# Kernel tuning notes

Hardware: AMD Instinct MI355X
Metric: run time of the kernel (lower is better)

## Reference

```python
import jax, jax.numpy as jnp
import numpy as np

N, F, A = 50000, 128, 128

def setup_inputs() -> dict:
    key = jax.random.key(0)
    ks = jax.random.split(key, 20)
    r = lambda i, shape: jax.random.normal(ks[i], shape, dtype=jnp.float32)
    w = lambda i, shape: jax.random.normal(ks[i], shape, dtype=jnp.float32) * 0.05
    return {
        "feat": r(0, (N, F)),
        "mu": r(1, (N, F, 3)),
        "T0": r(2, (N,)),
        "T1": r(3, (N, 3)),
        "T2": r(4, (N, 3, 3)),
        "T3": r(5, (N, 3, 3, 3)),
        # denseq: Dense(F,F,swish) -> Dense(F,F). Weights stored [in,out].
        "Wq1": w(6, (F, F)), "bq1": jnp.zeros((F,), jnp.float32),
        "Wq2": w(7, (F, F)), "bq2": jnp.zeros((F,), jnp.float32),
        "WT1": w(8, (F, F)),  # dense_T1, no bias
        "WT2": w(9, (F, F)),  # dense_T2, no bias
        "WT3": w(10, (F, F)), # dense_T3, no bias
        # dense_s: Dense(F,F,swish) -> Dense(F,A)
        "Ws1": w(11, (F, F)), "bs1": jnp.zeros((F,), jnp.float32),
        "Ws2": w(12, (F, A)), "bs2": jnp.zeros((A,), jnp.float32),
        "Wv": w(13, (F, A)),  # dense_v, no bias
    }

def reference(feat, mu, T0, T1, T2, T3,
              Wq1, bq1, Wq2, bq2, WT1, WT2, WT3,
              Ws1, bs1, Ws2, bs2, Wv):
    silu = jax.nn.silu  # swish
    # M0 = denseq(feat): [N, F]
    M0 = silu(feat @ Wq1 + bq1) @ Wq2 + bq2
    # M1/M2/M3: linear over feature dim of mu [N, F, 3]
    M1 = jnp.einsum('nfc,fg->ngc', mu, WT1)
    M2 = jnp.einsum('nfc,fg->ngc', mu, WT2)
    M3 = jnp.einsum('nfc,fg->ngc', mu, WT3)
    # scalar channel
    ms = jnp.sum(M1 * T1[:, None, :], axis=-1) + T0[:, None] * M0          # T1, T0 terms
    ms = ms + jnp.einsum('nfi,nfj,nij->nf', M2, M2, T2)                    # quadrupole . T2
    ms = ms + jnp.einsum('nfi,nfj,nfk,nijk->nf', M3, M3, M3, T3)           # octupole . T3
    # vector channel [N, F, 3]
    mv = T1[:, None, :] * M0[..., None]
    mv = mv + jnp.einsum('nij,nfj->nfi', T2, M1)
    mv = mv + jnp.einsum('nijk,nfj,nfk->nfi', T3, M2, M2)
    # output projections
    mv_out = jnp.einsum('nfc,fa->nac', mv, Wv)                             # [N, A, 3]
    ms_out = silu(ms @ Ws1 + bs1) @ Ws2 + bs2                              # [N, A]
    return ms_out, mv_out
```

## Files before the change

### kernel.cpp

```cpp
#include <hip/hip_runtime.h>
#include <cstdint>

#define N_NODES 50000
#define TILE 32
#define NBLK ((N_NODES + TILE - 1) / TILE)

typedef __bf16 bf16x8 __attribute__((ext_vector_type(8)));
typedef unsigned short ushort8_t __attribute__((ext_vector_type(8)));
typedef float f32x4 __attribute__((ext_vector_type(4)));

__device__ __forceinline__ unsigned short f2bf(float x) {
  union { float f; uint32_t u; } v; v.f = x;
  uint32_t r = v.u + 0x7FFFu + ((v.u >> 16) & 1u);
  return (unsigned short)(r >> 16);
}

__device__ __forceinline__ float fast_silu(float x) {
  return x / (1.0f + __expf(-x));
}

__global__ __launch_bounds__(256) void prep_weights(
    const float* __restrict__ Wq1, const float* __restrict__ Wq2,
    const float* __restrict__ WT1, const float* __restrict__ WT2,
    const float* __restrict__ WT3, const float* __restrict__ Ws1,
    const float* __restrict__ Ws2, const float* __restrict__ Wv,
    unsigned short* __restrict__ ws) {
  int tid = blockIdx.x * 256 + threadIdx.x;
  int w = tid >> 11;
  int rest = tid & 2047;
  int c = rest >> 8;
  int kt = (rest >> 6) & 3;
  int lane = rest & 63;
  int g = (lane & 15) + 16 * c;
  int k0 = kt * 32 + (lane >> 4) * 8;
  const float* srcs[8] = {Wq1, Wq2, WT1, WT2, WT3, Ws1, Ws2, Wv};
  const float* src = srcs[w];
  union { unsigned short u[8]; uint4 v; } o;
#pragma unroll
  for (int j = 0; j < 8; ++j) o.u[j] = f2bf(src[(k0 + j) * 128 + g]);
  *(uint4*)(ws + (size_t)w * 16384 + (size_t)rest * 8) = o.v;
}

__device__ __forceinline__ bf16x8 ldB(const unsigned short* __restrict__ wg,
                                      int c, int kt, int lane) {
  return __builtin_bit_cast(
      bf16x8, *(const ushort8_t*)(wg + (((c * 4 + kt) * 64 + lane)) * 8));
}

__device__ __forceinline__ void gemm16g(const unsigned short* __restrict__ sA,
                                        const unsigned short* __restrict__ wg,
                                        int lane, int cb, f32x4 acc[2][2]) {
  const int m = lane & 15, q = lane >> 4;
  const f32x4 vzero = {0.f, 0.f, 0.f, 0.f};
#pragma unroll
  for (int rt = 0; rt < 2; ++rt)
#pragma unroll
    for (int cc = 0; cc < 2; ++cc) acc[rt][cc] = vzero;
#pragma unroll
  for (int kt = 0; kt < 4; ++kt) {
    const int k0 = q * 8 + kt * 32;
    bf16x8 a0 = __builtin_bit_cast(bf16x8, *(const ushort8_t*)(sA + m * 136 + k0));
    bf16x8 a1 = __builtin_bit_cast(bf16x8, *(const ushort8_t*)(sA + (m + 16) * 136 + k0));
#pragma unroll
    for (int cc = 0; cc < 2; ++cc) {
      bf16x8 b = ldB(wg, cb + cc, kt, lane);
      acc[0][cc] = __builtin_amdgcn_mfma_f32_16x16x32_bf16(a0, b, acc[0][cc], 0, 0, 0);
      acc[1][cc] = __builtin_amdgcn_mfma_f32_16x16x32_bf16(a1, b, acc[1][cc], 0, 0, 0);
    }
  }
}

__device__ __forceinline__ void gemm3g(const unsigned short* __restrict__ s0,
                                       const unsigned short* __restrict__ s1,
                                       const unsigned short* __restrict__ s2,
                                       const unsigned short* __restrict__ wg,
                                       int lane, int cb,
                                       f32x4 A1[2][2], f32x4 A2[2][2],
                                       f32x4 A3[2][2]) {
  const int m = lane & 15, q = lane >> 4;
  const f32x4 vzero = {0.f, 0.f, 0.f, 0.f};
#pragma unroll
  for (int rt = 0; rt < 2; ++rt)
#pragma unroll
    for (int cc = 0; cc < 2; ++cc) {
      A1[rt][cc] = vzero; A2[rt][cc] = vzero; A3[rt][cc] = vzero;
    }
#pragma unroll
  for (int kt = 0; kt < 4; ++kt) {
    const int k0 = q * 8 + kt * 32;
    bf16x8 a00 = __builtin_bit_cast(bf16x8, *(const ushort8_t*)(s0 + m * 136 + k0));
    bf16x8 a01 = __builtin_bit_cast(bf16x8, *(const ushort8_t*)(s0 + (m + 16) * 136 + k0));
    bf16x8 a10 = __builtin_bit_cast(bf16x8, *(const ushort8_t*)(s1 + m * 136 + k0));
    bf16x8 a11 = __builtin_bit_cast(bf16x8, *(const ushort8_t*)(s1 + (m + 16) * 136 + k0));
    bf16x8 a20 = __builtin_bit_cast(bf16x8, *(const ushort8_t*)(s2 + m * 136 + k0));
    bf16x8 a21 = __builtin_bit_cast(bf16x8, *(const ushort8_t*)(s2 + (m + 16) * 136 + k0));
#pragma unroll
    for (int cc = 0; cc < 2; ++cc) {
      bf16x8 b = ldB(wg, cb + cc, kt, lane);
      A1[0][cc] = __builtin_amdgcn_mfma_f32_16x16x32_bf16(a00, b, A1[0][cc], 0, 0, 0);
      A1[1][cc] = __builtin_amdgcn_mfma_f32_16x16x32_bf16(a01, b, A1[1][cc], 0, 0, 0);
      A2[0][cc] = __builtin_amdgcn_mfma_f32_16x16x32_bf16(a10, b, A2[0][cc], 0, 0, 0);
      A2[1][cc] = __builtin_amdgcn_mfma_f32_16x16x32_bf16(a11, b, A2[1][cc], 0, 0, 0);
      A3[0][cc] = __builtin_amdgcn_mfma_f32_16x16x32_bf16(a20, b, A3[0][cc], 0, 0, 0);
      A3[1][cc] = __builtin_amdgcn_mfma_f32_16x16x32_bf16(a21, b, A3[1][cc], 0, 0, 0);
    }
  }
}

__global__ __launch_bounds__(256, 2) void multipole_main(
    const float* __restrict__ feat, const float* __restrict__ mu,
    const float* __restrict__ T0g, const float* __restrict__ T1g,
    const float* __restrict__ T2g, const float* __restrict__ T3g,
    const float* __restrict__ bq1, const float* __restrict__ bq2,
    const float* __restrict__ bs1, const float* __restrict__ bs2,
    const unsigned short* __restrict__ ws, float* __restrict__ out) {
  __shared__ unsigned short sXmain[TILE * 136];
  __shared__ unsigned short sXmu[3][TILE * 136];
  __shared__ float sT[TILE][47];

  const int t = threadIdx.x;
  const int lane = t & 63, wv = t >> 6;
  const int m = lane & 15, q = lane >> 4;
  const int cb = wv * 2;
  const int nodeBase = blockIdx.x * TILE;

  {
    int node = t >> 3, f0 = (t & 7) * 16;
    int gn = nodeBase + node;
    union { unsigned short u[16]; uint4 v[2]; } buf;
    if (gn < N_NODES) {
      const float4* p = (const float4*)(feat + (size_t)gn * 128 + f0);
      float xs[16];
#pragma unroll
      for (int i = 0; i < 4; ++i) *(float4*)(xs + 4 * i) = p[i];
#pragma unroll
      for (int i = 0; i < 16; ++i) buf.u[i] = f2bf(xs[i]);
    } else {
#pragma unroll
      for (int i = 0; i < 16; ++i) buf.u[i] = 0;
    }
    uint4* dst = (uint4*)&sXmain[node * 136 + f0];
    dst[0] = buf.v[0]; dst[1] = buf.v[1];
  }

  {
    int node = t >> 3, f0 = (t & 7) * 16;
    int gn = nodeBase + node;
    union { unsigned short u[16]; uint4 v[2]; } b3[3];
    if (gn < N_NODES) {
      const float4* p = (const float4*)(mu + ((size_t)gn * 128 + f0) * 3);
      float xs[48];
#pragma unroll
      for (int i = 0; i < 12; ++i) *(float4*)(xs + 4 * i) = p[i];
#pragma unroll
      for (int i = 0; i < 16; ++i) {
        b3[0].u[i] = f2bf(xs[i * 3 + 0]);
        b3[1].u[i] = f2bf(xs[i * 3 + 1]);
        b3[2].u[i] = f2bf(xs[i * 3 + 2]);
      }
    } else {
#pragma unroll
      for (int ch = 0; ch < 3; ++ch)
#pragma unroll
        for (int i = 0; i < 16; ++i) b3[ch].u[i] = 0;
    }
#pragma unroll
    for (int ch = 0; ch < 3; ++ch) {
      uint4* dst = (uint4*)&sXmu[ch][node * 136 + f0];
      dst[0] = b3[ch].v[0]; dst[1] = b3[ch].v[1];
    }
  }

  if (t < TILE) {
    int n = nodeBase + t;
    bool val = n < N_NODES;
    float t0 = val ? T0g[n] : 0.f;
    float t1[3], t2[9], t3[27];
#pragma unroll
    for (int i = 0; i < 3; ++i) t1[i] = val ? T1g[n * 3 + i] : 0.f;
#pragma unroll
    for (int i = 0; i < 9; ++i) t2[i] = val ? T2g[n * 9 + i] : 0.f;
#pragma unroll
    for (int i = 0; i < 27; ++i) t3[i] = val ? T3g[n * 27 + i] : 0.f;
    float* Tr = sT[t];
    Tr[0] = t0;
    Tr[1] = t1[0]; Tr[2] = t1[1]; Tr[3] = t1[2];
#pragma unroll
    for (int i = 0; i < 9; ++i) Tr[4 + i] = t2[i];
    Tr[13] = t2[0]; Tr[14] = t2[1] + t2[3]; Tr[15] = t2[2] + t2[6];
    Tr[16] = t2[4]; Tr[17] = t2[5] + t2[7]; Tr[18] = t2[8];
    Tr[19] = t3[0];
    Tr[20] = t3[1] + t3[3] + t3[9];
    Tr[21] = t3[2] + t3[6] + t3[18];
    Tr[22] = t3[4] + t3[10] + t3[12];
    Tr[23] = t3[5] + t3[7] + t3[11] + t3[15] + t3[19] + t3[21];
    Tr[24] = t3[8] + t3[20] + t3[24];
    Tr[25] = t3[13];
    Tr[26] = t3[14] + t3[16] + t3[22];
    Tr[27] = t3[17] + t3[23] + t3[25];
    Tr[28] = t3[26];
#pragma unroll
    for (int i = 0; i < 3; ++i) {
      const float* b = t3 + 9 * i;
      float* d = Tr + 29 + 6 * i;
      d[0] = b[0]; d[1] = b[1] + b[3]; d[2] = b[2] + b[6];
      d[3] = b[4]; d[4] = b[5] + b[7]; d[5] = b[8];
    }
  }
  __syncthreads();

  f32x4 A1[2][2], A2[2][2], A3[2][2];
  float msv[2][2][4];
  float mvv[3][2][2][4];

  gemm16g(sXmain, ws, lane, cb, A1);
  float b0 = bq1[cb * 16 + m], b1 = bq1[cb * 16 + 16 + m];
  __syncthreads();
#pragma unroll
  for (int rt = 0; rt < 2; ++rt)
#pragma unroll
    for (int ri = 0; ri < 4; ++ri) {
      int lrow = rt * 16 + q * 4 + ri;
#pragma unroll
      for (int cc = 0; cc < 2; ++cc) {
        float h = fast_silu(A1[rt][cc][ri] + (cc ? b1 : b0));
        sXmain[lrow * 136 + (cb + cc) * 16 + m] = f2bf(h);
      }
    }
  __syncthreads();

  gemm16g(sXmain, ws + 1 * 16384, lane, cb, A1);
  {
    float bb0 = bq2[cb * 16 + m], bb1 = bq2[cb * 16 + 16 + m];
#pragma unroll
    for (int rt = 0; rt < 2; ++rt)
#pragma unroll
      for (int ri = 0; ri < 4; ++ri) {
        const float* Tr = sT[rt * 16 + q * 4 + ri];
        float t0 = Tr[0], ta = Tr[1], tb = Tr[2], tc = Tr[3];
#pragma unroll
        for (int cc = 0; cc < 2; ++cc) {
          float m0 = A1[rt][cc][ri] + (cc ? bb1 : bb0);
          msv[rt][cc][ri] = t0 * m0;
          mvv[0][rt][cc][ri] = ta * m0;
          mvv[1][rt][cc][ri] = tb * m0;
          mvv[2][rt][cc][ri] = tc * m0;
        }
      }
  }

#pragma unroll
  for (int ch = 0; ch < 3; ++ch) {
    gemm16g(sXmu[ch], ws + 2 * 16384, lane, cb, A1);
#pragma unroll
    for (int rt = 0; rt < 2; ++rt)
#pragma unroll
      for (int ri = 0; ri < 4; ++ri) {
        const float* Tr = sT[rt * 16 + q * 4 + ri];
        float t1c = Tr[1 + ch];
        float u0 = Tr[4 + 0 + ch], u1 = Tr[4 + 3 + ch], u2 = Tr[4 + 6 + ch];
#pragma unroll
        for (int cc = 0; cc < 2; ++cc) {
          float v = A1[rt][cc][ri];
          msv[rt][cc][ri] += t1c * v;
          mvv[0][rt][cc][ri] += u0 * v;
          mvv[1][rt][cc][ri] += u1 * v;
          mvv[2][rt][cc][ri] += u2 * v;
        }
      }
  }

  gemm16g(sXmu[0], ws + 4 * 16384, lane, cb, A1);
  gemm16g(sXmu[1], ws + 4 * 16384, lane, cb, A2);
  gemm16g(sXmu[2], ws + 4 * 16384, lane, cb, A3);
#pragma unroll
  for (int rt = 0; rt < 2; ++rt)
#pragma unroll
    for (int ri = 0; ri < 4; ++ri) {
      const float* Cp = sT[rt * 16 + q * 4 + ri] + 19;
      float c0 = Cp[0], c1 = Cp[1], c2 = Cp[2], c3 = Cp[3], c4 = Cp[4];
      float c5 = Cp[5], c6 = Cp[6], c7 = Cp[7], c8 = Cp[8], c9 = Cp[9];
#pragma unroll
      for (int cc = 0; cc < 2; ++cc) {
        float u0 = A1[rt][cc][ri], u1 = A2[rt][cc][ri], u2 = A3[rt][cc][ri];
        float Q0 = u0 * u0, Q1 = u0 * u1, Q2 = u0 * u2;
        float Q3 = u1 * u1, Q4 = u1 * u2, Q5 = u2 * u2;
        msv[rt][cc][ri] += c0 * (Q0 * u0) + c1 * (Q0 * u1) + c2 * (Q0 * u2) +
                           c3 * (Q1 * u1) + c4 * (Q1 * u2) + c5 * (Q2 * u2) +
                           c6 * (Q3 * u1) + c7 * (Q3 * u2) + c8 * (Q4 * u2) +
                           c9 * (Q5 * u2);
      }
    }

  gemm16g(sXmu[0], ws + 3 * 16384, lane, cb, A1);
  gemm16g(sXmu[1], ws + 3 * 16384, lane, cb, A2);
  gemm16g(sXmu[2], ws + 3 * 16384, lane, cb, A3);
#pragma unroll
  for (int rt = 0; rt < 2; ++rt)
#pragma unroll
    for (int ri = 0; ri < 4; ++ri) {
      const float* Tr = sT[rt * 16 + q * 4 + ri];
      const float* q2 = Tr + 13;
      const float* d3 = Tr + 29;
      float q20 = q2[0], q21 = q2[1], q22 = q2[2], q23 = q2[3], q24 = q2[4], q25 = q2[5];
#pragma unroll
      for (int cc = 0; cc < 2; ++cc) {
        float v0 = A1[rt][cc][ri], v1 = A2[rt][cc][ri], v2 = A3[rt][cc][ri];
        float P0 = v0 * v0, P1 = v0 * v1, P2 = v0 * v2;
        float P3 = v1 * v1, P4 = v1 * v2, P5 = v2 * v2;
        msv[rt][cc][ri] += q20 * P0 + q21 * P1 + q22 * P2 + q23 * P3 + q24 * P4 + q25 * P5;
        mvv[0][rt][cc][ri] += d3[0] * P0 + d3[1] * P1 + d3[2] * P2 + d3[3] * P3 + d3[4] * P4 + d3[5] * P5;
        mvv[1][rt][cc][ri] += d3[6] * P0 + d3[7] * P1 + d3[8] * P2 + d3[9] * P3 + d3[10] * P4 + d3[11] * P5;
        mvv[2][rt][cc][ri] += d3[12] * P0 + d3[13] * P1 + d3[14] * P2 + d3[15] * P3 + d3[16] * P4 + d3[17] * P5;
      }
    }
  __syncthreads();

#pragma unroll
  for (int rt = 0; rt < 2; ++rt)
#pragma unroll
    for (int ri = 0; ri < 4; ++ri) {
      int lrow = rt * 16 + q * 4 + ri;
#pragma unroll
      for (int cc = 0; cc < 2; ++cc) {
        int col = (cb + cc) * 16 + m;
        sXmain[lrow * 136 + col] = f2bf(msv[rt][cc][ri]);
        sXmu[0][lrow * 136 + col] = f2bf(mvv[0][rt][cc][ri]);
        sXmu[1][lrow * 136 + col] = f2bf(mvv[1][rt][cc][ri]);
        sXmu[2][lrow * 136 + col] = f2bf(mvv[2][rt][cc][ri]);
      }
    }
  __syncthreads();

  gemm16g(sXmain, ws + 5 * 16384, lane, cb, A1);
  {
    float s0 = bs1[cb * 16 + m], s1 = bs1[cb * 16 + 16 + m];
    __syncthreads();
#pragma unroll
    for (int rt = 0; rt < 2; ++rt)
#pragma unroll
      for (int ri = 0; ri < 4; ++ri) {
        int lrow = rt * 16 + q * 4 + ri;
#pragma unroll
        for (int cc = 0; cc < 2; ++cc) {
          float g = fast_silu(A1[rt][cc][ri] + (cc ? s1 : s0));
          sXmain[lrow * 136 + (cb + cc) * 16 + m] = f2bf(g);
        }
      }
  }
  __syncthreads();

  gemm16g(sXmain, ws + 6 * 16384, lane, cb, A1);
  {
    float s0 = bs2[cb * 16 + m], s1 = bs2[cb * 16 + 16 + m];
#pragma unroll
    for (int rt = 0; rt < 2; ++rt)
#pragma unroll
      for (int ri = 0; ri < 4; ++ri) {
        int grow = nodeBase + rt * 16 + q * 4 + ri;
        if (grow < N_NODES) {
#pragma unroll
          for (int cc = 0; cc < 2; ++cc) {
            int col = (cb + cc) * 16 + m;
            out[(size_t)grow * 128 + col] = A1[rt][cc][ri] + (cc ? s1 : s0);
          }
        }
      }
  }

  float* out2 = out + (size_t)N_NODES * 128;
  gemm3g(sXmu[0], sXmu[1], sXmu[2], ws + 7 * 16384, lane, cb, A1, A2, A3);
#pragma unroll
  for (int rt = 0; rt < 2; ++rt)
#pragma unroll
    for (int ri = 0; ri < 4; ++ri) {
      int grow = nodeBase + rt * 16 + q * 4 + ri;
      if (grow < N_NODES) {
#pragma unroll
        for (int cc = 0; cc < 2; ++cc) {
          int col = (cb + cc) * 16 + m;
          float* p = out2 + ((size_t)grow * 128 + col) * 3;
          p[0] = A1[rt][cc][ri];
          p[1] = A2[rt][cc][ri];
          p[2] = A3[rt][cc][ri];
        }
      }
    }
}

extern "C" void kernel_launch(void* const* d_in, const int* in_sizes, int n_in,
                              void* d_out, int out_size, void* d_ws, size_t ws_size,
                              hipStream_t stream) {
  const float* feat = (const float*)d_in[0];
  const float* mu   = (const float*)d_in[1];
  const float* T0   = (const float*)d_in[2];
  const float* T1   = (const float*)d_in[3];
  const float* T2   = (const float*)d_in[4];
  const float* T3   = (const float*)d_in[5];
  const float* Wq1  = (const float*)d_in[6];
  const float* bq1  = (const float*)d_in[7];
  const float* Wq2  = (const float*)d_in[8];
  const float* bq2  = (const float*)d_in[9];
  const float* WT1  = (const float*)d_in[10];
  const float* WT2  = (const float*)d_in[11];
  const float* WT3  = (const float*)d_in[12];
  const float* Ws1  = (const float*)d_in[13];
  const float* bs1  = (const float*)d_in[14];
  const float* Ws2  = (const float*)d_in[15];
  const float* bs2  = (const float*)d_in[16];
  const float* Wv   = (const float*)d_in[17];
  unsigned short* ws = (unsigned short*)d_ws;
  float* out = (float*)d_out;

  prep_weights<<<64, 256, 0, stream>>>(Wq1, Wq2, WT1, WT2, WT3, Ws1, Ws2, Wv, ws);
  multipole_main<<<NBLK, 256, 0, stream>>>(feat, mu, T0, T1, T2, T3,
                                           bq1, bq2, bs1, bs2, ws, out);
}
```

Before: 307.6 us.

## Batch weight loads in GEMMs, merge per-channel GEMMs, use nontemporal global access

Three ideas are combined. The GEMM helpers now load all B fragments (and, in gemm16g, all A fragments) up front so memory latency can overlap the MFMA chain. The three per-channel gemm16g calls for the WT1, WT2 and WT3 products become single gemm3g calls that share weight loads across channels, with the T1/T2 epilogue rewritten to match. Streaming input loads and output stores become nontemporal to reduce cache pollution, at the cost of more live registers, which may lower occupancy.

```diff
diff --git a/kernel.cpp b/kernel.cpp
--- a/kernel.cpp
+++ b/kernel.cpp
@@ -47,27 +47,38 @@
       bf16x8, *(const ushort8_t*)(wg + (((c * 4 + kt) * 64 + lane)) * 8));
 }
 
+__device__ __forceinline__ bf16x8 ldA(const unsigned short* __restrict__ sA,
+                                      int row, int k0) {
+  return __builtin_bit_cast(bf16x8, *(const ushort8_t*)(sA + row * 136 + k0));
+}
+
 __device__ __forceinline__ void gemm16g(const unsigned short* __restrict__ sA,
                                         const unsigned short* __restrict__ wg,
                                         int lane, int cb, f32x4 acc[2][2]) {
   const int m = lane & 15, q = lane >> 4;
-  const f32x4 vzero = {0.f, 0.f, 0.f, 0.f};
-#pragma unroll
-  for (int rt = 0; rt < 2; ++rt)
-#pragma unroll
-    for (int cc = 0; cc < 2; ++cc) acc[rt][cc] = vzero;
+  bf16x8 b[2][4], a0[4], a1[4];
+#pragma unroll
+  for (int cc = 0; cc < 2; ++cc)
+#pragma unroll
+    for (int kt = 0; kt < 4; ++kt) b[cc][kt] = ldB(wg, cb + cc, kt, lane);
 #pragma unroll
   for (int kt = 0; kt < 4; ++kt) {
     const int k0 = q * 8 + kt * 32;
-    bf16x8 a0 = __builtin_bit_cast(bf16x8, *(const ushort8_t*)(sA + m * 136 + k0));
-    bf16x8 a1 = __builtin_bit_cast(bf16x8, *(const ushort8_t*)(sA + (m + 16) * 136 + k0));
+    a0[kt] = ldA(sA, m, k0);
+    a1[kt] = ldA(sA, m + 16, k0);
+  }
+  const f32x4 vzero = {0.f, 0.f, 0.f, 0.f};
+#pragma unroll
+  for (int rt = 0; rt < 2; ++rt)
+#pragma unroll
+    for (int cc = 0; cc < 2; ++cc) acc[rt][cc] = vzero;
+#pragma unroll
+  for (int kt = 0; kt < 4; ++kt)
 #pragma unroll
     for (int cc = 0; cc < 2; ++cc) {
-      bf16x8 b = ldB(wg, cb + cc, kt, lane);
-      acc[0][cc] = __builtin_amdgcn_mfma_f32_16x16x32_bf16(a0, b, acc[0][cc], 0, 0, 0);
-      acc[1][cc] = __builtin_amdgcn_mfma_f32_16x16x32_bf16(a1, b, acc[1][cc], 0, 0, 0);
-    }
-  }
+      acc[0][cc] = __builtin_amdgcn_mfma_f32_16x16x32_bf16(a0[kt], b[cc][kt], acc[0][cc], 0, 0, 0);
+      acc[1][cc] = __builtin_amdgcn_mfma_f32_16x16x32_bf16(a1[kt], b[cc][kt], acc[1][cc], 0, 0, 0);
+    }
 }
 
 __device__ __forceinline__ void gemm3g(const unsigned short* __restrict__ s0,
@@ -78,6 +89,11 @@
                                        f32x4 A1[2][2], f32x4 A2[2][2],
                                        f32x4 A3[2][2]) {
   const int m = lane & 15, q = lane >> 4;
+  bf16x8 b[2][4];
+#pragma unroll
+  for (int cc = 0; cc < 2; ++cc)
+#pragma unroll
+    for (int kt = 0; kt < 4; ++kt) b[cc][kt] = ldB(wg, cb + cc, kt, lane);
   const f32x4 vzero = {0.f, 0.f, 0.f, 0.f};
 #pragma unroll
   for (int rt = 0; rt < 2; ++rt)
@@ -88,21 +104,20 @@
 #pragma unroll
   for (int kt = 0; kt < 4; ++kt) {
     const int k0 = q * 8 + kt * 32;
-    bf16x8 a00 = __builtin_bit_cast(bf16x8, *(const ushort8_t*)(s0 + m * 136 + k0));
-    bf16x8 a01 = __builtin_bit_cast(bf16x8, *(const ushort8_t*)(s0 + (m + 16) * 136 + k0));
-    bf16x8 a10 = __builtin_bit_cast(bf16x8, *(const ushort8_t*)(s1 + m * 136 + k0));
-    bf16x8 a11 = __builtin_bit_cast(bf16x8, *(const ushort8_t*)(s1 + (m + 16) * 136 + k0));
-    bf16x8 a20 = __builtin_bit_cast(bf16x8, *(const ushort8_t*)(s2 + m * 136 + k0));
-    bf16x8 a21 = __builtin_bit_cast(bf16x8, *(const ushort8_t*)(s2 + (m + 16) * 136 + k0));
+    bf16x8 a00 = ldA(s0, m, k0);
+    bf16x8 a01 = ldA(s0, m + 16, k0);
+    bf16x8 a10 = ldA(s1, m, k0);
+    bf16x8 a11 = ldA(s1, m + 16, k0);
+    bf16x8 a20 = ldA(s2, m, k0);
+    bf16x8 a21 = ldA(s2, m + 16, k0);
 #pragma unroll
     for (int cc = 0; cc < 2; ++cc) {
-      bf16x8 b = ldB(wg, cb + cc, kt, lane);
-      A1[0][cc] = __builtin_amdgcn_mfma_f32_16x16x32_bf16(a00, b, A1[0][cc], 0, 0, 0);
-      A1[1][cc] = __builtin_amdgcn_mfma_f32_16x16x32_bf16(a01, b, A1[1][cc], 0, 0, 0);
-      A2[0][cc] = __builtin_amdgcn_mfma_f32_16x16x32_bf16(a10, b, A2[0][cc], 0, 0, 0);
-      A2[1][cc] = __builtin_amdgcn_mfma_f32_16x16x32_bf16(a11, b, A2[1][cc], 0, 0, 0);
-      A3[0][cc] = __builtin_amdgcn_mfma_f32_16x16x32_bf16(a20, b, A3[0][cc], 0, 0, 0);
-      A3[1][cc] = __builtin_amdgcn_mfma_f32_16x16x32_bf16(a21, b, A3[1][cc], 0, 0, 0);
+      A1[0][cc] = __builtin_amdgcn_mfma_f32_16x16x32_bf16(a00, b[cc][kt], A1[0][cc], 0, 0, 0);
+      A1[1][cc] = __builtin_amdgcn_mfma_f32_16x16x32_bf16(a01, b[cc][kt], A1[1][cc], 0, 0, 0);
+      A2[0][cc] = __builtin_amdgcn_mfma_f32_16x16x32_bf16(a10, b[cc][kt], A2[0][cc], 0, 0, 0);
+      A2[1][cc] = __builtin_amdgcn_mfma_f32_16x16x32_bf16(a11, b[cc][kt], A2[1][cc], 0, 0, 0);
+      A3[0][cc] = __builtin_amdgcn_mfma_f32_16x16x32_bf16(a20, b[cc][kt], A3[0][cc], 0, 0, 0);
+      A3[1][cc] = __builtin_amdgcn_mfma_f32_16x16x32_bf16(a21, b[cc][kt], A3[1][cc], 0, 0, 0);
     }
   }
 }
@@ -129,10 +144,10 @@
     int gn = nodeBase + node;
     union { unsigned short u[16]; uint4 v[2]; } buf;
     if (gn < N_NODES) {
-      const float4* p = (const float4*)(feat + (size_t)gn * 128 + f0);
+      const f32x4* p = (const f32x4*)(feat + (size_t)gn * 128 + f0);
       float xs[16];
 #pragma unroll
-      for (int i = 0; i < 4; ++i) *(float4*)(xs + 4 * i) = p[i];
+      for (int i = 0; i < 4; ++i) *(f32x4*)(xs + 4 * i) = __builtin_nontemporal_load(p + i);
 #pragma unroll
       for (int i = 0; i < 16; ++i) buf.u[i] = f2bf(xs[i]);
     } else {
@@ -148,10 +163,10 @@
     int gn = nodeBase + node;
     union { unsigned short u[16]; uint4 v[2]; } b3[3];
     if (gn < N_NODES) {
-      const float4* p = (const float4*)(mu + ((size_t)gn * 128 + f0) * 3);
+      const f32x4* p = (const f32x4*)(mu + ((size_t)gn * 128 + f0) * 3);
       float xs[48];
 #pragma unroll
-      for (int i = 0; i < 12; ++i) *(float4*)(xs + 4 * i) = p[i];
+      for (int i = 0; i < 12; ++i) *(f32x4*)(xs + 4 * i) = __builtin_nontemporal_load(p + i);
 #pragma unroll
       for (int i = 0; i < 16; ++i) {
         b3[0].u[i] = f2bf(xs[i * 3 + 0]);
@@ -174,14 +189,14 @@
   if (t < TILE) {
     int n = nodeBase + t;
     bool val = n < N_NODES;
-    float t0 = val ? T0g[n] : 0.f;
+    float t0 = val ? __builtin_nontemporal_load(T0g + n) : 0.f;
     float t1[3], t2[9], t3[27];
 #pragma unroll
-    for (int i = 0; i < 3; ++i) t1[i] = val ? T1g[n * 3 + i] : 0.f;
-#pragma unroll
-    for (int i = 0; i < 9; ++i) t2[i] = val ? T2g[n * 9 + i] : 0.f;
-#pragma unroll
-    for (int i = 0; i < 27; ++i) t3[i] = val ? T3g[n * 27 + i] : 0.f;
+    for (int i = 0; i < 3; ++i) t1[i] = val ? __builtin_nontemporal_load(T1g + n * 3 + i) : 0.f;
+#pragma unroll
+    for (int i = 0; i < 9; ++i) t2[i] = val ? __builtin_nontemporal_load(T2g + n * 9 + i) : 0.f;
+#pragma unroll
+    for (int i = 0; i < 27; ++i) t3[i] = val ? __builtin_nontemporal_load(T3g + n * 27 + i) : 0.f;
     float* Tr = sT[t];
     Tr[0] = t0;
     Tr[1] = t1[0]; Tr[2] = t1[1]; Tr[3] = t1[2];
@@ -249,30 +264,23 @@
       }
   }
 
-#pragma unroll
-  for (int ch = 0; ch < 3; ++ch) {
-    gemm16g(sXmu[ch], ws + 2 * 16384, lane, cb, A1);
-#pragma unroll
-    for (int rt = 0; rt < 2; ++rt)
-#pragma unroll
-      for (int ri = 0; ri < 4; ++ri) {
-        const float* Tr = sT[rt * 16 + q * 4 + ri];
-        float t1c = Tr[1 + ch];
-        float u0 = Tr[4 + 0 + ch], u1 = Tr[4 + 3 + ch], u2 = Tr[4 + 6 + ch];
-#pragma unroll
-        for (int cc = 0; cc < 2; ++cc) {
-          float v = A1[rt][cc][ri];
-          msv[rt][cc][ri] += t1c * v;
-          mvv[0][rt][cc][ri] += u0 * v;
-          mvv[1][rt][cc][ri] += u1 * v;
-          mvv[2][rt][cc][ri] += u2 * v;
-        }
-      }
-  }
-
-  gemm16g(sXmu[0], ws + 4 * 16384, lane, cb, A1);
-  gemm16g(sXmu[1], ws + 4 * 16384, lane, cb, A2);
-  gemm16g(sXmu[2], ws + 4 * 16384, lane, cb, A3);
+  gemm3g(sXmu[0], sXmu[1], sXmu[2], ws + 2 * 16384, lane, cb, A1, A2, A3);
+#pragma unroll
+  for (int rt = 0; rt < 2; ++rt)
+#pragma unroll
+    for (int ri = 0; ri < 4; ++ri) {
+      const float* Tr = sT[rt * 16 + q * 4 + ri];
+#pragma unroll
+      for (int cc = 0; cc < 2; ++cc) {
+        float v0 = A1[rt][cc][ri], v1 = A2[rt][cc][ri], v2 = A3[rt][cc][ri];
+        msv[rt][cc][ri] += Tr[1] * v0 + Tr[2] * v1 + Tr[3] * v2;
+        mvv[0][rt][cc][ri] += Tr[4] * v0 + Tr[5] * v1 + Tr[6] * v2;
+        mvv[1][rt][cc][ri] += Tr[7] * v0 + Tr[8] * v1 + Tr[9] * v2;
+        mvv[2][rt][cc][ri] += Tr[10] * v0 + Tr[11] * v1 + Tr[12] * v2;
+      }
+    }
+
+  gemm3g(sXmu[0], sXmu[1], sXmu[2], ws + 4 * 16384, lane, cb, A1, A2, A3);
 #pragma unroll
   for (int rt = 0; rt < 2; ++rt)
 #pragma unroll
@@ -292,9 +300,7 @@
       }
     }
 
-  gemm16g(sXmu[0], ws + 3 * 16384, lane, cb, A1);
-  gemm16g(sXmu[1], ws + 3 * 16384, lane, cb, A2);
-  gemm16g(sXmu[2], ws + 3 * 16384, lane, cb, A3);
+  gemm3g(sXmu[0], sXmu[1], sXmu[2], ws + 3 * 16384, lane, cb, A1, A2, A3);
 #pragma unroll
   for (int rt = 0; rt < 2; ++rt)
 #pragma unroll
@@ -362,7 +368,8 @@
 #pragma unroll
           for (int cc = 0; cc < 2; ++cc) {
             int col = (cb + cc) * 16 + m;
-            out[(size_t)grow * 128 + col] = A1[rt][cc][ri] + (cc ? s1 : s0);
+            __builtin_nontemporal_store(A1[rt][cc][ri] + (cc ? s1 : s0),
+                                        out + (size_t)grow * 128 + col);
           }
         }
       }
@@ -380,9 +387,9 @@
         for (int cc = 0; cc < 2; ++cc) {
           int col = (cb + cc) * 16 + m;
           float* p = out2 + ((size_t)grow * 128 + col) * 3;
-          p[0] = A1[rt][cc][ri];
-          p[1] = A2[rt][cc][ri];
-          p[2] = A3[rt][cc][ri];
+          __builtin_nontemporal_store(A1[rt][cc][ri], p + 0);
+          __builtin_nontemporal_store(A2[rt][cc][ri], p + 1);
+          __builtin_nontemporal_store(A3[rt][cc][ri], p + 2);
         }
       }
     }
```

Measured after the change: 300.2 us. 2.4% less time.
